# Kernel optimization log

Hardware: AMD Instinct MI355X
Metric: run time of the kernel (lower is better)

## Reference

```python
import jax, jax.numpy as jnp
import numpy as np

OBS_DIM, HIDDEN, OUT = 64, 128, 128
BATCH = 524288


def _mlp(x, W1, b1, W2, b2, W3, b3):
    # torch Linear: y = x @ W.T + b
    h = jax.nn.relu(x @ W1.T + b1)
    h = jax.nn.relu(h @ W2.T + b2)
    return h @ W3.T + b3


def setup_inputs() -> dict:
    key = jax.random.key(0)
    ks = jax.random.split(key, 13)

    def lin(k, fan_out, fan_in):
        bound = 1.0 / np.sqrt(fan_in)
        kw, kb = jax.random.split(k)
        W = jax.random.uniform(kw, (fan_out, fan_in), jnp.float32, -bound, bound)
        b = jax.random.uniform(kb, (fan_out,), jnp.float32, -bound, bound)
        return W, b

    tW1, tb1 = lin(ks[0], HIDDEN, OBS_DIM)
    tW2, tb2 = lin(ks[1], HIDDEN, HIDDEN)
    tW3, tb3 = lin(ks[2], OUT, HIDDEN)
    pW1, pb1 = lin(ks[3], HIDDEN, OBS_DIM)
    pW2, pb2 = lin(ks[4], HIDDEN, HIDDEN)
    pW3, pb3 = lin(ks[5], OUT, HIDDEN)
    obs = jax.random.normal(ks[6], (BATCH, OBS_DIM), jnp.float32)
    return {
        "obs": obs,
        "reward_mean": jnp.zeros((1,), jnp.float32),
        "reward_m2": jnp.zeros((1,), jnp.float32),
        "reward_count": jnp.zeros((1,), jnp.float32),
        "tW1": tW1, "tb1": tb1, "tW2": tW2, "tb2": tb2, "tW3": tW3, "tb3": tb3,
        "pW1": pW1, "pb1": pb1, "pW2": pW2, "pb2": pb2, "pW3": pW3, "pb3": pb3,
    }


def reference(obs, reward_mean, reward_m2, reward_count,
              tW1, tb1, tW2, tb2, tW3, tb3,
              pW1, pb1, pW2, pb2, pW3, pb3):
    # compute_bonus: per-sample MSE between fixed target net and predictor net
    tgt = _mlp(obs, tW1, tb1, tW2, tb2, tW3, tb3)
    pred = _mlp(obs, pW1, pb1, pW2, pb2, pW3, pb3)
    rewards = jnp.mean((tgt - pred) ** 2, axis=-1)  # (batch,)

    # normalize_rewards: sequential Welford over every element ==
    # single batch Welford + Chan merge with running stats (exact same math)
    n = jnp.float32(rewards.shape[0])
    batch_mean = jnp.mean(rewards)
    batch_m2 = jnp.sum((rewards - batch_mean) ** 2)
    new_count = reward_count + n                      # (1,)
    delta = batch_mean - reward_mean                  # (1,)
    new_mean = reward_mean + delta * n / new_count
    new_m2 = reward_m2 + batch_m2 + delta * delta * reward_count * n / new_count
    std = jnp.where(new_count > 1.0,
                    jnp.sqrt(new_m2 / (new_count - 1.0)),
                    jnp.ones_like(new_mean))
    normalized = (rewards - new_mean) / (std + 1e-8)  # (batch,)
    return normalized
```

## Files before the change

kernel.cpp:

```cpp
#include <hip/hip_runtime.h>
#include <stdint.h>

#define BATCH 524288
#define OBSD  64

typedef short v8s __attribute__((ext_vector_type(8)));
typedef float v4f __attribute__((ext_vector_type(4)));

union U8 { int4 i4; v8s v; uint32_t u[4]; };

__device__ __forceinline__ uint32_t bf16rne(float f) {
  uint32_t u = __float_as_uint(f);
  return (u + 0x7fffu + ((u >> 16) & 1u)) >> 16;
}
__device__ __forceinline__ uint32_t pk2(float a, float b) {
  uint32_t r;
  asm("v_cvt_pk_bf16_f32 %0, %1, %2" : "=v"(r) : "v"(a), "v"(b));
  return r;
}

__global__ void rnd_prep(const float* __restrict__ tW1, const float* __restrict__ tW2,
                         const float* __restrict__ tW3, const float* __restrict__ pW1,
                         const float* __restrict__ pW2, const float* __restrict__ pW3,
                         uint16_t* __restrict__ Wall, float* __restrict__ sums) {
  int i = blockIdx.x * 256 + threadIdx.x;
  if (i < 2) sums[i] = 0.0f;
  float v;
  if      (i < 8192)  v = tW1[i];
  else if (i < 24576) v = tW2[i - 8192];
  else if (i < 40960) v = tW3[i - 24576];
  else if (i < 49152) v = pW1[i - 40960];
  else if (i < 65536) v = pW2[i - 49152];
  else                v = -pW3[i - 65536];
  Wall[i] = (uint16_t)bf16rne(v);
}

__global__ __launch_bounds__(256, 3) void rnd_main(
    const float* __restrict__ obs, const uint16_t* __restrict__ Wall,
    const float* __restrict__ b1t, const float* __restrict__ b2t,
    const float* __restrict__ b1p, const float* __restrict__ b2p,
    const float* __restrict__ b3t, const float* __restrict__ b3p,
    float* __restrict__ rewards, float* __restrict__ sums) {
  __shared__ __align__(16) uint16_t Wbuf[128 * 136];
  __shared__ float bs[4], bss[4];
  const int t    = threadIdx.x;
  const int lane = t & 63;
  const int wv   = t >> 6;
  const int n    = lane & 15;
  const int q    = lane >> 4;
  const int s0   = (blockIdx.x * 4 + wv) * 32;

  auto stage64 = [&](const uint16_t* src) {
    #pragma unroll
    for (int i = 0; i < 4; ++i) {
      int g = i * 256 + t;
      int d = g >> 3, c = g & 7;
      U8 u; u.i4 = *(const int4*)(src + g * 8);
      *(int4*)(Wbuf + d * 72 + c * 8) = u.i4;
    }
  };
  auto stage128 = [&](const uint16_t* src) {
    #pragma unroll
    for (int i = 0; i < 8; ++i) {
      int g = i * 256 + t;
      int d = g >> 4, c = g & 15;
      U8 u; u.i4 = *(const int4*)(src + g * 8);
      *(int4*)(Wbuf + d * 136 + c * 8) = u.i4;
    }
  };
  auto afragL = [&](int Kp, int rt, int ks) -> v8s {
    U8 u; u.i4 = *(const int4*)(Wbuf + (rt * 16 + n) * Kp + ks * 32 + q * 8);
    return u.v;
  };

  float4 of[8];
  #pragma unroll
  for (int ct = 0; ct < 2; ++ct)
    #pragma unroll
    for (int ks = 0; ks < 2; ++ks) {
      const float* p = obs + (size_t)(s0 + ct * 16 + n) * OBSD + ks * 32 + q * 8;
      of[(ct * 2 + ks) * 2 + 0] = *(const float4*)p;
      of[(ct * 2 + ks) * 2 + 1] = *(const float4*)(p + 4);
    }
  stage64(Wall + 0);

  v8s obf[2][2];
  #pragma unroll
  for (int ct = 0; ct < 2; ++ct)
    #pragma unroll
    for (int ks = 0; ks < 2; ++ks) {
      float4 f0 = of[(ct * 2 + ks) * 2 + 0];
      float4 f1 = of[(ct * 2 + ks) * 2 + 1];
      U8 u;
      u.u[0] = pk2(f0.x, f0.y); u.u[1] = pk2(f0.z, f0.w);
      u.u[2] = pk2(f1.x, f1.y); u.u[3] = pk2(f1.z, f1.w);
      obf[ct][ks] = u.v;
    }

  auto bias_init = [&](const float* b, v4f (&acc)[8][2]) {
    #pragma unroll
    for (int rt = 0; rt < 8; ++rt) {
      float4 bv = *(const float4*)(b + rt * 16 + q * 4);
      v4f c; c[0] = bv.x; c[1] = bv.y; c[2] = bv.z; c[3] = bv.w;
      acc[rt][0] = c; acc[rt][1] = c;
    }
  };
  auto pack_out = [&](v4f (&acc)[8][2], uint32_t (&P)[8][2][2]) {
    #pragma unroll
    for (int rt = 0; rt < 8; ++rt)
      #pragma unroll
      for (int ct = 0; ct < 2; ++ct) {
        v4f a = acc[rt][ct];
        a[0] = fmaxf(a[0], 0.f); a[1] = fmaxf(a[1], 0.f);
        a[2] = fmaxf(a[2], 0.f); a[3] = fmaxf(a[3], 0.f);
        P[rt][ct][0] = pk2(a[0], a[1]);
        P[rt][ct][1] = pk2(a[2], a[3]);
      }
  };
  auto bfrag_from = [&](uint32_t (&P)[8][2][2], int ks, int ct) -> v8s {
    uint32_t x0 = P[2 * ks][ct][0],     x1 = P[2 * ks][ct][1];
    uint32_t y0 = P[2 * ks + 1][ct][0], y1 = P[2 * ks + 1][ct][1];
    asm("v_permlane32_swap_b32 %0, %1" : "+v"(x0), "+v"(y0));
    asm("v_permlane16_swap_b32 %0, %1" : "+v"(x0), "+v"(y0));
    asm("v_permlane32_swap_b32 %0, %1" : "+v"(x1), "+v"(y1));
    asm("v_permlane16_swap_b32 %0, %1" : "+v"(x1), "+v"(y1));
    U8 u; u.u[0] = x0; u.u[1] = x1; u.u[2] = y0; u.u[3] = y1;
    return u.v;
  };

  auto layer1 = [&](const float* b, uint32_t (&P)[8][2][2]) {
    v4f acc[8][2];
    bias_init(b, acc);
    #pragma unroll
    for (int ks = 0; ks < 2; ++ks) {
      #pragma unroll
      for (int rt = 0; rt < 8; ++rt) {
        v8s af = afragL(72, rt, ks);
        acc[rt][0] = __builtin_amdgcn_mfma_f32_16x16x32_bf16(af, obf[0][ks], acc[rt][0], 0, 0, 0);
        acc[rt][1] = __builtin_amdgcn_mfma_f32_16x16x32_bf16(af, obf[1][ks], acc[rt][1], 0, 0, 0);
      }
    }
    pack_out(acc, P);
  };
  auto layer2 = [&](const float* b, uint32_t (&Pin)[8][2][2], uint32_t (&Pout)[8][2][2]) {
    v4f acc[8][2];
    bias_init(b, acc);
    #pragma unroll
    for (int ks = 0; ks < 4; ++ks) {
      v8s bf0 = bfrag_from(Pin, ks, 0), bf1 = bfrag_from(Pin, ks, 1);
      #pragma unroll
      for (int rt = 0; rt < 8; ++rt) {
        v8s af = afragL(136, rt, ks);
        acc[rt][0] = __builtin_amdgcn_mfma_f32_16x16x32_bf16(af, bf0, acc[rt][0], 0, 0, 0);
        acc[rt][1] = __builtin_amdgcn_mfma_f32_16x16x32_bf16(af, bf1, acc[rt][1], 0, 0, 0);
      }
    }
    pack_out(acc, Pout);
  };

  uint32_t Pa[8][2][2];
  uint32_t Pt[8][2][2];

  __syncthreads();
  layer1(b1t, Pa);          __syncthreads();
  stage128(Wall + 8192);    __syncthreads();
  layer2(b2t, Pa, Pt);      __syncthreads();
  stage64(Wall + 40960);    __syncthreads();
  layer1(b1p, Pa);          __syncthreads();
  stage128(Wall + 49152);   __syncthreads();
  layer2(b2p, Pa, Pa);      __syncthreads();

  v4f acc[8][2];
  #pragma unroll
  for (int rt = 0; rt < 8; ++rt) {
    float4 bt = *(const float4*)(b3t + rt * 16 + q * 4);
    float4 bp = *(const float4*)(b3p + rt * 16 + q * 4);
    v4f c; c[0] = bt.x - bp.x; c[1] = bt.y - bp.y; c[2] = bt.z - bp.z; c[3] = bt.w - bp.w;
    acc[rt][0] = c; acc[rt][1] = c;
  }
  stage128(Wall + 24576);   __syncthreads();
  #pragma unroll
  for (int ks = 0; ks < 4; ++ks) {
    v8s bf0 = bfrag_from(Pt, ks, 0), bf1 = bfrag_from(Pt, ks, 1);
    #pragma unroll
    for (int rt = 0; rt < 8; ++rt) {
      v8s af = afragL(136, rt, ks);
      acc[rt][0] = __builtin_amdgcn_mfma_f32_16x16x32_bf16(af, bf0, acc[rt][0], 0, 0, 0);
      acc[rt][1] = __builtin_amdgcn_mfma_f32_16x16x32_bf16(af, bf1, acc[rt][1], 0, 0, 0);
    }
  }
  __syncthreads();
  stage128(Wall + 65536);   __syncthreads();
  #pragma unroll
  for (int ks = 0; ks < 4; ++ks) {
    v8s bf0 = bfrag_from(Pa, ks, 0), bf1 = bfrag_from(Pa, ks, 1);
    #pragma unroll
    for (int rt = 0; rt < 8; ++rt) {
      v8s af = afragL(136, rt, ks);
      acc[rt][0] = __builtin_amdgcn_mfma_f32_16x16x32_bf16(af, bf0, acc[rt][0], 0, 0, 0);
      acc[rt][1] = __builtin_amdgcn_mfma_f32_16x16x32_bf16(af, bf1, acc[rt][1], 0, 0, 0);
    }
  }

  float p0 = 0.f, p1 = 0.f;
  #pragma unroll
  for (int rt = 0; rt < 8; ++rt) {
    v4f a0 = acc[rt][0], a1 = acc[rt][1];
    p0 += a0[0]*a0[0] + a0[1]*a0[1] + a0[2]*a0[2] + a0[3]*a0[3];
    p1 += a1[0]*a1[0] + a1[1]*a1[1] + a1[2]*a1[2] + a1[3]*a1[3];
  }
  p0 += __shfl_xor(p0, 32); p0 += __shfl_xor(p0, 16);
  p1 += __shfl_xor(p1, 32); p1 += __shfl_xor(p1, 16);
  float r0 = p0 * (1.0f / 128.0f), r1 = p1 * (1.0f / 128.0f);
  if (q == 0) {
    rewards[s0 + n]      = r0;
    rewards[s0 + 16 + n] = r1;
  }
  float s = r0 + r1, ss = r0 * r0 + r1 * r1;
  s  += __shfl_xor(s, 8);  s  += __shfl_xor(s, 4);  s  += __shfl_xor(s, 2);  s  += __shfl_xor(s, 1);
  ss += __shfl_xor(ss, 8); ss += __shfl_xor(ss, 4); ss += __shfl_xor(ss, 2); ss += __shfl_xor(ss, 1);
  if (lane == 0) { bs[wv] = s; bss[wv] = ss; }
  __syncthreads();
  if (t == 0) {
    atomicAdd(&sums[0], bs[0] + bs[1] + bs[2] + bs[3]);
    atomicAdd(&sums[1], bss[0] + bss[1] + bss[2] + bss[3]);
  }
}

__global__ void rnd_norm(const float* __restrict__ rewards, const float* __restrict__ sums,
                         const float* __restrict__ rm, const float* __restrict__ rm2,
                         const float* __restrict__ rc, float* __restrict__ out) {
  float S = sums[0], SS = sums[1];
  float nb = (float)BATCH;
  float bm = S / nb;
  float bm2 = SS - nb * bm * bm;
  float cnt = rc[0];
  float newc = cnt + nb;
  float delta = bm - rm[0];
  float newmean = rm[0] + delta * nb / newc;
  float newm2 = rm2[0] + bm2 + delta * delta * cnt * nb / newc;
  float sd = (newc > 1.f) ? sqrtf(newm2 / (newc - 1.f)) : 1.f;
  float inv = 1.f / (sd + 1e-8f);
  int i = (blockIdx.x * 256 + threadIdx.x) * 4;
  float4 r = *(const float4*)(rewards + i);
  float4 o;
  o.x = (r.x - newmean) * inv; o.y = (r.y - newmean) * inv;
  o.z = (r.z - newmean) * inv; o.w = (r.w - newmean) * inv;
  *(float4*)(out + i) = o;
}

extern "C" void kernel_launch(void* const* d_in, const int* in_sizes, int n_in,
                              void* d_out, int out_size, void* d_ws, size_t ws_size,
                              hipStream_t stream) {
  const float* obs = (const float*)d_in[0];
  const float* rm  = (const float*)d_in[1];
  const float* rm2 = (const float*)d_in[2];
  const float* rc  = (const float*)d_in[3];
  const float* tW1 = (const float*)d_in[4];
  const float* tb1 = (const float*)d_in[5];
  const float* tW2 = (const float*)d_in[6];
  const float* tb2 = (const float*)d_in[7];
  const float* tW3 = (const float*)d_in[8];
  const float* tb3 = (const float*)d_in[9];
  const float* pW1 = (const float*)d_in[10];
  const float* pb1 = (const float*)d_in[11];
  const float* pW2 = (const float*)d_in[12];
  const float* pb2 = (const float*)d_in[13];
  const float* pW3 = (const float*)d_in[14];
  const float* pb3 = (const float*)d_in[15];

  float*    sums    = (float*)d_ws;
  float*    rewards = (float*)((char*)d_ws + 256);
  uint16_t* Wall    = (uint16_t*)((char*)d_ws + 256 + (size_t)BATCH * 4);

  rnd_prep<<<320, 256, 0, stream>>>(tW1, tW2, tW3, pW1, pW2, pW3, Wall, sums);
  rnd_main<<<BATCH / 128, 256, 0, stream>>>(obs, Wall, tb1, tb2, pb1, pb2, tb3, pb3,
                                            rewards, sums);
  rnd_norm<<<BATCH / 1024, 256, 0, stream>>>(rewards, sums, rm, rm2, rc, (float*)d_out);
}
```

Measured before the change: 336.5 us.

## Stage both layer-1 weights together and batch global loads before LDS stores

The shared weight buffer is enlarged so that the target and predictor layer-1 weights can be staged at once. Both layer-1 passes now run back to back, which removes one staging phase and two barriers. The staging code now issues all global loads into registers before any LDS writes, and addressing uses precomputed base pointers, to expose more memory-level parallelism. The larger LDS footprint and extra live registers could lower occupancy under the 3-blocks-per-SM launch bound.

```diff
diff --git a/kernel.cpp b/kernel.cpp
--- a/kernel.cpp
+++ b/kernel.cpp
@@ -41,7 +41,7 @@
     const float* __restrict__ b1p, const float* __restrict__ b2p,
     const float* __restrict__ b3t, const float* __restrict__ b3p,
     float* __restrict__ rewards, float* __restrict__ sums) {
-  __shared__ __align__(16) uint16_t Wbuf[128 * 136];
+  __shared__ __align__(16) uint16_t Wbuf[128 * 144];
   __shared__ float bs[4], bss[4];
   const int t    = threadIdx.x;
   const int lane = t & 63;
@@ -50,28 +50,10 @@
   const int q    = lane >> 4;
   const int s0   = (blockIdx.x * 4 + wv) * 32;
 
-  auto stage64 = [&](const uint16_t* src) {
-    #pragma unroll
-    for (int i = 0; i < 4; ++i) {
-      int g = i * 256 + t;
-      int d = g >> 3, c = g & 7;
-      U8 u; u.i4 = *(const int4*)(src + g * 8);
-      *(int4*)(Wbuf + d * 72 + c * 8) = u.i4;
-    }
-  };
-  auto stage128 = [&](const uint16_t* src) {
-    #pragma unroll
-    for (int i = 0; i < 8; ++i) {
-      int g = i * 256 + t;
-      int d = g >> 4, c = g & 15;
-      U8 u; u.i4 = *(const int4*)(src + g * 8);
-      *(int4*)(Wbuf + d * 136 + c * 8) = u.i4;
-    }
-  };
-  auto afragL = [&](int Kp, int rt, int ks) -> v8s {
-    U8 u; u.i4 = *(const int4*)(Wbuf + (rt * 16 + n) * Kp + ks * 32 + q * 8);
-    return u.v;
-  };
+  uint16_t*       sw1      = Wbuf + (t >> 3) * 72  + (t & 7)  * 8;
+  uint16_t*       sw2      = Wbuf + (t >> 4) * 136 + (t & 15) * 8;
+  const uint16_t* abase72  = Wbuf + n * 72  + q * 8;
+  const uint16_t* abase136 = Wbuf + n * 136 + q * 8;
 
   float4 of[8];
   #pragma unroll
@@ -82,8 +64,15 @@
       of[(ct * 2 + ks) * 2 + 0] = *(const float4*)p;
       of[(ct * 2 + ks) * 2 + 1] = *(const float4*)(p + 4);
     }
-  stage64(Wall + 0);
-
+  int4 w1a[4], w1b[4];
+  {
+    const uint16_t* g0 = Wall + t * 8;
+    const uint16_t* g1 = Wall + 40960 + t * 8;
+    #pragma unroll
+    for (int i = 0; i < 4; ++i) w1a[i] = *(const int4*)(g0 + i * 2048);
+    #pragma unroll
+    for (int i = 0; i < 4; ++i) w1b[i] = *(const int4*)(g1 + i * 2048);
+  }
   v8s obf[2][2];
   #pragma unroll
   for (int ct = 0; ct < 2; ++ct)
@@ -96,6 +85,27 @@
       u.u[2] = pk2(f1.x, f1.y); u.u[3] = pk2(f1.z, f1.w);
       obf[ct][ks] = u.v;
     }
+  #pragma unroll
+  for (int i = 0; i < 4; ++i) *(int4*)(sw1 + i * 2304) = w1a[i];
+  #pragma unroll
+  for (int i = 0; i < 4; ++i) *(int4*)(sw1 + 9216 + i * 2304) = w1b[i];
+
+  auto stage128 = [&](const uint16_t* src) {
+    const uint16_t* g = src + t * 8;
+    int4 tmp[8];
+    #pragma unroll
+    for (int i = 0; i < 8; ++i) tmp[i] = *(const int4*)(g + i * 2048);
+    #pragma unroll
+    for (int i = 0; i < 8; ++i) *(int4*)(sw2 + i * 2176) = tmp[i];
+  };
+  auto afrag72 = [&](int sub, int rt, int ks) -> v8s {
+    U8 u; u.i4 = *(const int4*)(abase72 + sub + rt * 1152 + ks * 32);
+    return u.v;
+  };
+  auto afrag136 = [&](int rt, int ks) -> v8s {
+    U8 u; u.i4 = *(const int4*)(abase136 + rt * 2176 + ks * 32);
+    return u.v;
+  };
 
   auto bias_init = [&](const float* b, v4f (&acc)[8][2]) {
     #pragma unroll
@@ -128,14 +138,14 @@
     return u.v;
   };
 
-  auto layer1 = [&](const float* b, uint32_t (&P)[8][2][2]) {
+  auto layer1 = [&](int sub, const float* b, uint32_t (&P)[8][2][2]) {
     v4f acc[8][2];
     bias_init(b, acc);
     #pragma unroll
     for (int ks = 0; ks < 2; ++ks) {
       #pragma unroll
       for (int rt = 0; rt < 8; ++rt) {
-        v8s af = afragL(72, rt, ks);
+        v8s af = afrag72(sub, rt, ks);
         acc[rt][0] = __builtin_amdgcn_mfma_f32_16x16x32_bf16(af, obf[0][ks], acc[rt][0], 0, 0, 0);
         acc[rt][1] = __builtin_amdgcn_mfma_f32_16x16x32_bf16(af, obf[1][ks], acc[rt][1], 0, 0, 0);
       }
@@ -150,7 +160,7 @@
       v8s bf0 = bfrag_from(Pin, ks, 0), bf1 = bfrag_from(Pin, ks, 1);
       #pragma unroll
       for (int rt = 0; rt < 8; ++rt) {
-        v8s af = afragL(136, rt, ks);
+        v8s af = afrag136(rt, ks);
         acc[rt][0] = __builtin_amdgcn_mfma_f32_16x16x32_bf16(af, bf0, acc[rt][0], 0, 0, 0);
         acc[rt][1] = __builtin_amdgcn_mfma_f32_16x16x32_bf16(af, bf1, acc[rt][1], 0, 0, 0);
       }
@@ -158,17 +168,17 @@
     pack_out(acc, Pout);
   };
 
+  uint32_t Pt[8][2][2];
   uint32_t Pa[8][2][2];
-  uint32_t Pt[8][2][2];
 
   __syncthreads();
-  layer1(b1t, Pa);          __syncthreads();
-  stage128(Wall + 8192);    __syncthreads();
-  layer2(b2t, Pa, Pt);      __syncthreads();
-  stage64(Wall + 40960);    __syncthreads();
-  layer1(b1p, Pa);          __syncthreads();
-  stage128(Wall + 49152);   __syncthreads();
-  layer2(b2p, Pa, Pa);      __syncthreads();
+  layer1(0,    b1t, Pt);
+  layer1(9216, b1p, Pa);   __syncthreads();
+  stage128(Wall + 8192);   __syncthreads();
+  layer2(b2t, Pt, Pt);     __syncthreads();
+  stage128(Wall + 49152);  __syncthreads();
+  layer2(b2p, Pa, Pa);     __syncthreads();
+  stage128(Wall + 24576);  __syncthreads();
 
   v4f acc[8][2];
   #pragma unroll
@@ -178,25 +188,24 @@
     v4f c; c[0] = bt.x - bp.x; c[1] = bt.y - bp.y; c[2] = bt.z - bp.z; c[3] = bt.w - bp.w;
     acc[rt][0] = c; acc[rt][1] = c;
   }
-  stage128(Wall + 24576);   __syncthreads();
   #pragma unroll
   for (int ks = 0; ks < 4; ++ks) {
     v8s bf0 = bfrag_from(Pt, ks, 0), bf1 = bfrag_from(Pt, ks, 1);
     #pragma unroll
     for (int rt = 0; rt < 8; ++rt) {
-      v8s af = afragL(136, rt, ks);
+      v8s af = afrag136(rt, ks);
       acc[rt][0] = __builtin_amdgcn_mfma_f32_16x16x32_bf16(af, bf0, acc[rt][0], 0, 0, 0);
       acc[rt][1] = __builtin_amdgcn_mfma_f32_16x16x32_bf16(af, bf1, acc[rt][1], 0, 0, 0);
     }
   }
   __syncthreads();
-  stage128(Wall + 65536);   __syncthreads();
+  stage128(Wall + 65536);  __syncthreads();
   #pragma unroll
   for (int ks = 0; ks < 4; ++ks) {
     v8s bf0 = bfrag_from(Pa, ks, 0), bf1 = bfrag_from(Pa, ks, 1);
     #pragma unroll
     for (int rt = 0; rt < 8; ++rt) {
-      v8s af = afragL(136, rt, ks);
+      v8s af = afrag136(rt, ks);
       acc[rt][0] = __builtin_amdgcn_mfma_f32_16x16x32_bf16(af, bf0, acc[rt][0], 0, 0, 0);
       acc[rt][1] = __builtin_amdgcn_mfma_f32_16x16x32_bf16(af, bf1, acc[rt][1], 0, 0, 0);
     }
```

Result: no change. 331.8 us (-1.4%).

## Make main kernel persistent with both W2 matrices resident in swizzled LDS

Applied to the files above, without the earlier changes.

The main kernel now runs 1024 blocks that each loop over four batch tiles instead of launching one block per tile. Both layer-2 weight matrices are staged once per block into 64KB of dynamic LDS with an XOR-style swizzle. Layers 1 and 3 read pre-fragmented weights straight from global memory, laid out by the prep kernel to match the MFMA operand order. This removes the repeated per-tile weight staging and the many barriers between layers, in exchange for lower occupancy (two blocks per CU), more cached global loads, and obs loads that are no longer overlapped with staging.

```diff
diff --git a/kernel.cpp b/kernel.cpp
--- a/kernel.cpp
+++ b/kernel.cpp
@@ -9,10 +9,6 @@
 
 union U8 { int4 i4; v8s v; uint32_t u[4]; };
 
-__device__ __forceinline__ uint32_t bf16rne(float f) {
-  uint32_t u = __float_as_uint(f);
-  return (u + 0x7fffu + ((u >> 16) & 1u)) >> 16;
-}
 __device__ __forceinline__ uint32_t pk2(float a, float b) {
   uint32_t r;
   asm("v_cvt_pk_bf16_f32 %0, %1, %2" : "=v"(r) : "v"(a), "v"(b));
@@ -23,80 +19,74 @@
                          const float* __restrict__ tW3, const float* __restrict__ pW1,
                          const float* __restrict__ pW2, const float* __restrict__ pW3,
                          uint16_t* __restrict__ Wall, float* __restrict__ sums) {
-  int i = blockIdx.x * 256 + threadIdx.x;
-  if (i < 2) sums[i] = 0.0f;
-  float v;
-  if      (i < 8192)  v = tW1[i];
-  else if (i < 24576) v = tW2[i - 8192];
-  else if (i < 40960) v = tW3[i - 24576];
-  else if (i < 49152) v = pW1[i - 40960];
-  else if (i < 65536) v = pW2[i - 49152];
-  else                v = -pW3[i - 65536];
-  Wall[i] = (uint16_t)bf16rne(v);
-}
-
-__global__ __launch_bounds__(256, 3) void rnd_main(
+  int g = blockIdx.x * 256 + threadIdx.x;
+  if (g < 2) sums[g] = 0.0f;
+  const float* src;
+  uint16_t* dst;
+  float sgn = 1.f;
+  if (g < 4096) {
+    src = (g < 2048) ? (tW2 + g * 8) : (pW2 + g * 8 - 16384);
+    dst = Wall + g * 8;
+  } else if (g < 6144) {
+    int u = g - 4096;
+    int m = u >> 10; u &= 1023;
+    int rt = u >> 7, ks = (u >> 6) & 1, lane = u & 63;
+    int n = lane & 15, qq = lane >> 4;
+    src = (m ? pW1 : tW1) + (rt * 16 + n) * 64 + ks * 32 + qq * 8;
+    dst = Wall + 32768 + m * 8192 + u * 8;
+  } else {
+    int u = g - 6144;
+    int m = u >> 11; u &= 2047;
+    int rt = u >> 8, ks = (u >> 6) & 3, lane = u & 63;
+    int n = lane & 15, qq = lane >> 4;
+    src = (m ? pW3 : tW3) + (rt * 16 + n) * 128 + ks * 32 + qq * 8;
+    sgn = m ? -1.f : 1.f;
+    dst = Wall + 49152 + m * 16384 + u * 8;
+  }
+  float4 f0 = *(const float4*)src, f1 = *(const float4*)(src + 4);
+  U8 u8;
+  u8.u[0] = pk2(sgn * f0.x, sgn * f0.y); u8.u[1] = pk2(sgn * f0.z, sgn * f0.w);
+  u8.u[2] = pk2(sgn * f1.x, sgn * f1.y); u8.u[3] = pk2(sgn * f1.z, sgn * f1.w);
+  *(int4*)dst = u8.i4;
+}
+
+__global__ __launch_bounds__(256, 2) void rnd_main(
     const float* __restrict__ obs, const uint16_t* __restrict__ Wall,
     const float* __restrict__ b1t, const float* __restrict__ b2t,
     const float* __restrict__ b1p, const float* __restrict__ b2p,
     const float* __restrict__ b3t, const float* __restrict__ b3p,
     float* __restrict__ rewards, float* __restrict__ sums) {
-  __shared__ __align__(16) uint16_t Wbuf[128 * 136];
-  __shared__ float bs[4], bss[4];
+  extern __shared__ uint16_t Wl[];
   const int t    = threadIdx.x;
   const int lane = t & 63;
   const int wv   = t >> 6;
   const int n    = lane & 15;
   const int q    = lane >> 4;
-  const int s0   = (blockIdx.x * 4 + wv) * 32;
-
-  auto stage64 = [&](const uint16_t* src) {
-    #pragma unroll
-    for (int i = 0; i < 4; ++i) {
-      int g = i * 256 + t;
-      int d = g >> 3, c = g & 7;
-      U8 u; u.i4 = *(const int4*)(src + g * 8);
-      *(int4*)(Wbuf + d * 72 + c * 8) = u.i4;
-    }
-  };
-  auto stage128 = [&](const uint16_t* src) {
-    #pragma unroll
-    for (int i = 0; i < 8; ++i) {
-      int g = i * 256 + t;
-      int d = g >> 4, c = g & 15;
-      U8 u; u.i4 = *(const int4*)(src + g * 8);
-      *(int4*)(Wbuf + d * 136 + c * 8) = u.i4;
-    }
-  };
-  auto afragL = [&](int Kp, int rt, int ks) -> v8s {
-    U8 u; u.i4 = *(const int4*)(Wbuf + (rt * 16 + n) * Kp + ks * 32 + q * 8);
+
+  {
+    uint16_t* wb = Wl + (t >> 4) * 128 + ((((t & 15) + (t >> 4)) & 15) << 3);
+    const uint16_t* gsrc = Wall + t * 8;
+    #pragma unroll
+    for (int m = 0; m < 2; ++m)
+      #pragma unroll
+      for (int i = 0; i < 8; ++i) {
+        U8 u; u.i4 = *(const int4*)(gsrc + m * 16384 + i * 2048);
+        *(int4*)(wb + m * 16384 + i * 2048) = u.i4;
+      }
+  }
+  const uint16_t* a2k0 = Wl + n * 128 + ((((0 * 4) + q + n) & 15) << 3);
+  const uint16_t* a2k1 = Wl + n * 128 + ((((1 * 4) + q + n) & 15) << 3);
+  const uint16_t* a2k2 = Wl + n * 128 + ((((2 * 4) + q + n) & 15) << 3);
+  const uint16_t* a2k3 = Wl + n * 128 + ((((3 * 4) + q + n) & 15) << 3);
+  const uint16_t* wb1 = Wall + 32768 + lane * 8;
+  const uint16_t* wb3 = Wall + 49152 + lane * 8;
+  __syncthreads();
+
+  auto afragW2 = [&](int m, int rt, int ks) -> v8s {
+    const uint16_t* b = (ks == 0) ? a2k0 : (ks == 1) ? a2k1 : (ks == 2) ? a2k2 : a2k3;
+    U8 u; u.i4 = *(const int4*)(b + m * 16384 + rt * 2048);
     return u.v;
   };
-
-  float4 of[8];
-  #pragma unroll
-  for (int ct = 0; ct < 2; ++ct)
-    #pragma unroll
-    for (int ks = 0; ks < 2; ++ks) {
-      const float* p = obs + (size_t)(s0 + ct * 16 + n) * OBSD + ks * 32 + q * 8;
-      of[(ct * 2 + ks) * 2 + 0] = *(const float4*)p;
-      of[(ct * 2 + ks) * 2 + 1] = *(const float4*)(p + 4);
-    }
-  stage64(Wall + 0);
-
-  v8s obf[2][2];
-  #pragma unroll
-  for (int ct = 0; ct < 2; ++ct)
-    #pragma unroll
-    for (int ks = 0; ks < 2; ++ks) {
-      float4 f0 = of[(ct * 2 + ks) * 2 + 0];
-      float4 f1 = of[(ct * 2 + ks) * 2 + 1];
-      U8 u;
-      u.u[0] = pk2(f0.x, f0.y); u.u[1] = pk2(f0.z, f0.w);
-      u.u[2] = pk2(f1.x, f1.y); u.u[3] = pk2(f1.z, f1.w);
-      obf[ct][ks] = u.v;
-    }
-
   auto bias_init = [&](const float* b, v4f (&acc)[8][2]) {
     #pragma unroll
     for (int rt = 0; rt < 8; ++rt) {
@@ -128,102 +118,111 @@
     return u.v;
   };
 
-  auto layer1 = [&](const float* b, uint32_t (&P)[8][2][2]) {
+  float sAcc = 0.f, ssAcc = 0.f;
+  #pragma unroll 1
+  for (int it = 0; it < 4; ++it) {
+    const int tile = it * 4096 + blockIdx.x * 4 + wv;
+    const int s0   = tile * 32;
+
+    v8s obf[2][2];
+    #pragma unroll
+    for (int ct = 0; ct < 2; ++ct)
+      #pragma unroll
+      for (int ks = 0; ks < 2; ++ks) {
+        const float* p = obs + (size_t)(s0 + ct * 16 + n) * OBSD + ks * 32 + q * 8;
+        float4 f0 = *(const float4*)p;
+        float4 f1 = *(const float4*)(p + 4);
+        U8 u;
+        u.u[0] = pk2(f0.x, f0.y); u.u[1] = pk2(f0.z, f0.w);
+        u.u[2] = pk2(f1.x, f1.y); u.u[3] = pk2(f1.z, f1.w);
+        obf[ct][ks] = u.v;
+      }
+
+    uint32_t Pt[8][2][2], Pa[8][2][2];
+    #pragma unroll
+    for (int m = 0; m < 2; ++m) {
+      v4f acc[8][2];
+      bias_init(m ? b1p : b1t, acc);
+      #pragma unroll
+      for (int ks = 0; ks < 2; ++ks)
+        #pragma unroll
+        for (int rt = 0; rt < 8; ++rt) {
+          U8 u; u.i4 = *(const int4*)(wb1 + m * 8192 + (rt * 2 + ks) * 512);
+          acc[rt][0] = __builtin_amdgcn_mfma_f32_16x16x32_bf16(u.v, obf[0][ks], acc[rt][0], 0, 0, 0);
+          acc[rt][1] = __builtin_amdgcn_mfma_f32_16x16x32_bf16(u.v, obf[1][ks], acc[rt][1], 0, 0, 0);
+        }
+      pack_out(acc, m ? Pa : Pt);
+    }
+    #pragma unroll
+    for (int m = 0; m < 2; ++m) {
+      uint32_t (&P)[8][2][2] = m ? Pa : Pt;
+      v4f acc[8][2];
+      bias_init(m ? b2p : b2t, acc);
+      #pragma unroll
+      for (int ks = 0; ks < 4; ++ks) {
+        v8s bf0 = bfrag_from(P, ks, 0), bf1 = bfrag_from(P, ks, 1);
+        #pragma unroll
+        for (int rt = 0; rt < 8; ++rt) {
+          v8s af = afragW2(m, rt, ks);
+          acc[rt][0] = __builtin_amdgcn_mfma_f32_16x16x32_bf16(af, bf0, acc[rt][0], 0, 0, 0);
+          acc[rt][1] = __builtin_amdgcn_mfma_f32_16x16x32_bf16(af, bf1, acc[rt][1], 0, 0, 0);
+        }
+      }
+      pack_out(acc, P);
+    }
     v4f acc[8][2];
-    bias_init(b, acc);
-    #pragma unroll
-    for (int ks = 0; ks < 2; ++ks) {
-      #pragma unroll
-      for (int rt = 0; rt < 8; ++rt) {
-        v8s af = afragL(72, rt, ks);
-        acc[rt][0] = __builtin_amdgcn_mfma_f32_16x16x32_bf16(af, obf[0][ks], acc[rt][0], 0, 0, 0);
-        acc[rt][1] = __builtin_amdgcn_mfma_f32_16x16x32_bf16(af, obf[1][ks], acc[rt][1], 0, 0, 0);
-      }
-    }
-    pack_out(acc, P);
-  };
-  auto layer2 = [&](const float* b, uint32_t (&Pin)[8][2][2], uint32_t (&Pout)[8][2][2]) {
-    v4f acc[8][2];
-    bias_init(b, acc);
-    #pragma unroll
-    for (int ks = 0; ks < 4; ++ks) {
-      v8s bf0 = bfrag_from(Pin, ks, 0), bf1 = bfrag_from(Pin, ks, 1);
-      #pragma unroll
-      for (int rt = 0; rt < 8; ++rt) {
-        v8s af = afragL(136, rt, ks);
-        acc[rt][0] = __builtin_amdgcn_mfma_f32_16x16x32_bf16(af, bf0, acc[rt][0], 0, 0, 0);
-        acc[rt][1] = __builtin_amdgcn_mfma_f32_16x16x32_bf16(af, bf1, acc[rt][1], 0, 0, 0);
-      }
-    }
-    pack_out(acc, Pout);
-  };
-
-  uint32_t Pa[8][2][2];
-  uint32_t Pt[8][2][2];
-
+    #pragma unroll
+    for (int rt = 0; rt < 8; ++rt) {
+      float4 bt = *(const float4*)(b3t + rt * 16 + q * 4);
+      float4 bp = *(const float4*)(b3p + rt * 16 + q * 4);
+      v4f c; c[0] = bt.x - bp.x; c[1] = bt.y - bp.y; c[2] = bt.z - bp.z; c[3] = bt.w - bp.w;
+      acc[rt][0] = c; acc[rt][1] = c;
+    }
+    #pragma unroll
+    for (int m = 0; m < 2; ++m) {
+      uint32_t (&P)[8][2][2] = m ? Pa : Pt;
+      #pragma unroll
+      for (int ks = 0; ks < 4; ++ks) {
+        v8s bf0 = bfrag_from(P, ks, 0), bf1 = bfrag_from(P, ks, 1);
+        #pragma unroll
+        for (int rt = 0; rt < 8; ++rt) {
+          U8 u; u.i4 = *(const int4*)(wb3 + m * 16384 + (rt * 4 + ks) * 512);
+          acc[rt][0] = __builtin_amdgcn_mfma_f32_16x16x32_bf16(u.v, bf0, acc[rt][0], 0, 0, 0);
+          acc[rt][1] = __builtin_amdgcn_mfma_f32_16x16x32_bf16(u.v, bf1, acc[rt][1], 0, 0, 0);
+        }
+      }
+    }
+
+    float p0 = 0.f, p1 = 0.f;
+    #pragma unroll
+    for (int rt = 0; rt < 8; ++rt) {
+      v4f a0 = acc[rt][0], a1 = acc[rt][1];
+      p0 += a0[0]*a0[0] + a0[1]*a0[1] + a0[2]*a0[2] + a0[3]*a0[3];
+      p1 += a1[0]*a1[0] + a1[1]*a1[1] + a1[2]*a1[2] + a1[3]*a1[3];
+    }
+    p0 += __shfl_xor(p0, 32); p0 += __shfl_xor(p0, 16);
+    p1 += __shfl_xor(p1, 32); p1 += __shfl_xor(p1, 16);
+    float r0 = p0 * (1.0f / 128.0f), r1 = p1 * (1.0f / 128.0f);
+    if (q == 0) {
+      rewards[s0 + n]      = r0;
+      rewards[s0 + 16 + n] = r1;
+    }
+    sAcc  += r0 + r1;
+    ssAcc += r0 * r0 + r1 * r1;
+  }
+
+  #pragma unroll
+  for (int d = 1; d < 64; d <<= 1) {
+    sAcc  += __shfl_xor(sAcc, d);
+    ssAcc += __shfl_xor(ssAcc, d);
+  }
   __syncthreads();
-  layer1(b1t, Pa);          __syncthreads();
-  stage128(Wall + 8192);    __syncthreads();
-  layer2(b2t, Pa, Pt);      __syncthreads();
-  stage64(Wall + 40960);    __syncthreads();
-  layer1(b1p, Pa);          __syncthreads();
-  stage128(Wall + 49152);   __syncthreads();
-  layer2(b2p, Pa, Pa);      __syncthreads();
-
-  v4f acc[8][2];
-  #pragma unroll
-  for (int rt = 0; rt < 8; ++rt) {
-    float4 bt = *(const float4*)(b3t + rt * 16 + q * 4);
-    float4 bp = *(const float4*)(b3p + rt * 16 + q * 4);
-    v4f c; c[0] = bt.x - bp.x; c[1] = bt.y - bp.y; c[2] = bt.z - bp.z; c[3] = bt.w - bp.w;
-    acc[rt][0] = c; acc[rt][1] = c;
-  }
-  stage128(Wall + 24576);   __syncthreads();
-  #pragma unroll
-  for (int ks = 0; ks < 4; ++ks) {
-    v8s bf0 = bfrag_from(Pt, ks, 0), bf1 = bfrag_from(Pt, ks, 1);
-    #pragma unroll
-    for (int rt = 0; rt < 8; ++rt) {
-      v8s af = afragL(136, rt, ks);
-      acc[rt][0] = __builtin_amdgcn_mfma_f32_16x16x32_bf16(af, bf0, acc[rt][0], 0, 0, 0);
-      acc[rt][1] = __builtin_amdgcn_mfma_f32_16x16x32_bf16(af, bf1, acc[rt][1], 0, 0, 0);
-    }
-  }
-  __syncthreads();
-  stage128(Wall + 65536);   __syncthreads();
-  #pragma unroll
-  for (int ks = 0; ks < 4; ++ks) {
-    v8s bf0 = bfrag_from(Pa, ks, 0), bf1 = bfrag_from(Pa, ks, 1);
-    #pragma unroll
-    for (int rt = 0; rt < 8; ++rt) {
-      v8s af = afragL(136, rt, ks);
-      acc[rt][0] = __builtin_amdgcn_mfma_f32_16x16x32_bf16(af, bf0, acc[rt][0], 0, 0, 0);
-      acc[rt][1] = __builtin_amdgcn_mfma_f32_16x16x32_bf16(af, bf1, acc[rt][1], 0, 0, 0);
-    }
-  }
-
-  float p0 = 0.f, p1 = 0.f;
-  #pragma unroll
-  for (int rt = 0; rt < 8; ++rt) {
-    v4f a0 = acc[rt][0], a1 = acc[rt][1];
-    p0 += a0[0]*a0[0] + a0[1]*a0[1] + a0[2]*a0[2] + a0[3]*a0[3];
-    p1 += a1[0]*a1[0] + a1[1]*a1[1] + a1[2]*a1[2] + a1[3]*a1[3];
-  }
-  p0 += __shfl_xor(p0, 32); p0 += __shfl_xor(p0, 16);
-  p1 += __shfl_xor(p1, 32); p1 += __shfl_xor(p1, 16);
-  float r0 = p0 * (1.0f / 128.0f), r1 = p1 * (1.0f / 128.0f);
-  if (q == 0) {
-    rewards[s0 + n]      = r0;
-    rewards[s0 + 16 + n] = r1;
-  }
-  float s = r0 + r1, ss = r0 * r0 + r1 * r1;
-  s  += __shfl_xor(s, 8);  s  += __shfl_xor(s, 4);  s  += __shfl_xor(s, 2);  s  += __shfl_xor(s, 1);
-  ss += __shfl_xor(ss, 8); ss += __shfl_xor(ss, 4); ss += __shfl_xor(ss, 2); ss += __shfl_xor(ss, 1);
-  if (lane == 0) { bs[wv] = s; bss[wv] = ss; }
+  float* red = (float*)Wl;
+  if (lane == 0) { red[wv] = sAcc; red[8 + wv] = ssAcc; }
   __syncthreads();
   if (t == 0) {
-    atomicAdd(&sums[0], bs[0] + bs[1] + bs[2] + bs[3]);
-    atomicAdd(&sums[1], bss[0] + bss[1] + bss[2] + bss[3]);
+    atomicAdd(&sums[0], 0.25f * (red[0] + red[1] + red[2] + red[3]));
+    atomicAdd(&sums[1], 0.25f * (red[8] + red[9] + red[10] + red[11]));
   }
 }
 
@@ -273,8 +272,11 @@
   float*    rewards = (float*)((char*)d_ws + 256);
   uint16_t* Wall    = (uint16_t*)((char*)d_ws + 256 + (size_t)BATCH * 4);
 
-  rnd_prep<<<320, 256, 0, stream>>>(tW1, tW2, tW3, pW1, pW2, pW3, Wall, sums);
-  rnd_main<<<BATCH / 128, 256, 0, stream>>>(obs, Wall, tb1, tb2, pb1, pb2, tb3, pb3,
-                                            rewards, sums);
+  (void)hipFuncSetAttribute((const void*)rnd_main,
+                            hipFuncAttributeMaxDynamicSharedMemorySize, 65536);
+
+  rnd_prep<<<40, 256, 0, stream>>>(tW1, tW2, tW3, pW1, pW2, pW3, Wall, sums);
+  rnd_main<<<1024, 256, 65536, stream>>>(obs, Wall, tb1, tb2, pb1, pb2, tb3, pb3,
+                                         rewards, sums);
   rnd_norm<<<BATCH / 1024, 256, 0, stream>>>(rewards, sums, rm, rm2, rc, (float*)d_out);
 }
```

Result: slower. 538.8 us (+60.1%).
